# Kernel tuning notes

Hardware: AMD Instinct MI355X
Metric: run time of the kernel (lower is better)

Reference implementation:

```python
import jax, jax.numpy as jnp
import numpy as np

N = 100000   # nodes
E = 600000   # directed edges (no self loops)
T = 128      # n_timestamps
DIMS = [128, 64, 32, 16]  # get_layer_dims(128, 3, 0.5)


def _glorot(key, din, dout):
    lim = float(np.sqrt(6.0 / (din + dout)))
    return jax.random.uniform(key, (din, dout), jnp.float32, -lim, lim)


def setup_inputs() -> dict:
    key = jax.random.key(0)
    ks = jax.random.split(key, 16)
    row = jax.random.randint(ks[0], (E,), 0, N, dtype=jnp.int32)
    off = jax.random.randint(ks[1], (E,), 1, N, dtype=jnp.int32)
    col = (row + off) % N  # guarantees no self loops
    edge_index = jnp.stack([row, col])
    x = jax.random.normal(ks[2], (N, T), dtype=jnp.float32)
    enc = [(DIMS[0], DIMS[1]), (DIMS[1], DIMS[2]), (DIMS[2], DIMS[3])]
    dec = [(DIMS[3], DIMS[2]), (DIMS[2], DIMS[1]), (DIMS[1], DIMS[0])]
    inp = {"x": x, "edge_index": edge_index}
    for i, (di, do) in enumerate(enc):
        inp[f"We{i+1}"] = _glorot(ks[3 + i], di, do)
        inp[f"be{i+1}"] = 0.01 * jax.random.normal(ks[6 + i], (do,), jnp.float32)
    for i, (di, do) in enumerate(dec):
        inp[f"Wd{i+1}"] = _glorot(ks[9 + i], di, do)
        inp[f"bd{i+1}"] = 0.01 * jax.random.normal(ks[12 + i], (do,), jnp.float32)
    return inp


def _with_self_loops(edge_index, n):
    ar = jnp.arange(n, dtype=edge_index.dtype)
    row = jnp.concatenate([edge_index[0], ar])
    col = jnp.concatenate([edge_index[1], ar])
    return row, col


def _deg_inv_sqrt(w, col, n):
    deg = jax.ops.segment_sum(w, col, num_segments=n)
    return jnp.where(deg > 0, jax.lax.rsqrt(deg), 0.0)


def _smooth_norm(edge_index, n):
    # gcn_norm: A_hat = A + I (fill 1), sym normalize D^-1/2 A_hat D^-1/2
    row, col = _with_self_loops(edge_index, n)
    w = jnp.ones(row.shape[0], jnp.float32)
    dinv = _deg_inv_sqrt(w, col, n)
    return row, col, dinv[row] * w * dinv[col]


def _sharp_norm(edge_index, n):
    # gcn_sharp: A_hat = -A + 2I, D_hat from (A + 2I), norm = D^-1/2 A_hat D^-1/2
    row, col = _with_self_loops(edge_index, n)
    e = edge_index.shape[1]
    wA = jnp.concatenate([-jnp.ones(e, jnp.float32), 2.0 * jnp.ones(n, jnp.float32)])
    wD = jnp.concatenate([jnp.ones(e, jnp.float32), 2.0 * jnp.ones(n, jnp.float32)])
    dinv = _deg_inv_sqrt(wD, col, n)
    return row, col, dinv[row] * wA * dinv[col]


def _conv(x, W, b, row, col, ew, n):
    # x -> lin -> gather source, scale by edge weight, scatter-add to target, + bias
    h = x @ W
    out = jax.ops.segment_sum(ew[:, None] * h[row], col, num_segments=n)
    return out + b


def reference(x, edge_index, We1, be1, We2, be2, We3, be3,
              Wd1, bd1, Wd2, bd2, Wd3, bd3):
    n = x.shape[0]
    sr, sc, sw = _smooth_norm(edge_index, n)   # encoder ('smooth')
    hr, hc, hw = _sharp_norm(edge_index, n)    # decoder ('sharp')
    # encoder: conv+ReLU x3
    h = jax.nn.relu(_conv(x, We1, be1, sr, sc, sw, n))
    h = jax.nn.relu(_conv(h, We2, be2, sr, sc, sw, n))
    z = jax.nn.relu(_conv(h, We3, be3, sr, sc, sw, n))
    # decoder: conv+ReLU x2, final conv without ReLU
    h = jax.nn.relu(_conv(z, Wd1, bd1, hr, hc, hw, n))
    h = jax.nn.relu(_conv(h, Wd2, bd2, hr, hc, hw, n))
    o = _conv(h, Wd3, bd3, hr, hc, hw, n)
    return o
```

## Files before the change

kernel.cpp:

```cpp
#include <hip/hip_runtime.h>


static inline int ceil_div(int a, int b) { return (a + b - 1) / b; }

#define SCAN_BLK 256
#define NBINS 128

typedef _Float16 f16;
typedef _Float16 f16x8 __attribute__((ext_vector_type(8)));
typedef float f32x4 __attribute__((ext_vector_type(4)));


__global__ void zero_kernel(int* __restrict__ p, int n) {
    int i = blockIdx.x * blockDim.x + threadIdx.x;
    if (i < n) p[i] = 0;
}


__global__ void deg_kernel(const int* __restrict__ col, int* __restrict__ deg, int E) {
    int e = blockIdx.x * blockDim.x + threadIdx.x;
    if (e < E) atomicAdd(&deg[col[e]], 1);
}


__global__ void hist_kernel(const int* __restrict__ deg, int* __restrict__ blockhist, int n) {
    __shared__ int lh[NBINS];
    if (threadIdx.x < NBINS) lh[threadIdx.x] = 0;
    __syncthreads();
    int i = blockIdx.x * SCAN_BLK + threadIdx.x;
    if (i < n) {
        int d = deg[i]; if (d >= NBINS) d = NBINS - 1;
        atomicAdd(&lh[d], 1);
    }
    __syncthreads();
    if (threadIdx.x < NBINS) blockhist[blockIdx.x * NBINS + threadIdx.x] = lh[threadIdx.x];
}

__global__ void binscan_kernel(int* __restrict__ blockhist, int* __restrict__ bintot, int nb) {
    __shared__ int s[512];
    int bin = blockIdx.x, t = threadIdx.x;
    int v = (t < nb) ? blockhist[t * NBINS + bin] : 0;
    s[t] = v;
    __syncthreads();
    for (int st = 1; st < 512; st <<= 1) {
        int a = (t >= st) ? s[t - st] : 0;
        __syncthreads();
        s[t] += a;
        __syncthreads();
    }
    if (t < nb) blockhist[t * NBINS + bin] = s[t] - v;
    if (t == 0) bintot[bin] = s[511];
}

__global__ void base_scan_kernel(const int* __restrict__ bintot, int* __restrict__ binbase,
                                 int* __restrict__ edgebase) {
    __shared__ int s[NBINS], se[NBINS];
    int t = threadIdx.x;
    int v = bintot[t];
    int ve = v * t;
    s[t] = v; se[t] = ve;
    __syncthreads();
    for (int st = 1; st < NBINS; st <<= 1) {
        int a = (t >= st) ? s[t - st] : 0;
        int ae = (t >= st) ? se[t - st] : 0;
        __syncthreads();
        s[t] += a; se[t] += ae;
        __syncthreads();
    }
    binbase[t] = s[t] - v;
    edgebase[t] = se[t] - ve;
}

__global__ void place_kernel(const int* __restrict__ deg, const int* __restrict__ blockhist,
                             const int* __restrict__ binbase, int* __restrict__ order,
                             int* __restrict__ slotof, int n) {
    __shared__ int lh[NBINS];
    if (threadIdx.x < NBINS) lh[threadIdx.x] = 0;
    __syncthreads();
    int i = blockIdx.x * SCAN_BLK + threadIdx.x;
    if (i < n) {
        int d = deg[i]; if (d >= NBINS) d = NBINS - 1;
        int r = atomicAdd(&lh[d], 1);
        int slot = binbase[d] + blockhist[blockIdx.x * NBINS + d] + r;
        order[slot] = i;
        slotof[i] = slot;
    }
}

__global__ void dinvp_offs_kernel(const int* __restrict__ deg, const int* __restrict__ order,
                                  const int* __restrict__ binbase, const int* __restrict__ edgebase,
                                  float* __restrict__ dinv_s, float* __restrict__ dinv_h,
                                  int* __restrict__ offs, int* __restrict__ cursor, int n, int E) {
    int s = blockIdx.x * blockDim.x + threadIdx.x;
    if (s < n) {
        int dd = deg[order[s]];
        float d = (float)dd;
        dinv_s[s] = rsqrtf(d + 1.0f);
        dinv_h[s] = rsqrtf(d + 2.0f);
        int o = edgebase[dd] + dd * (s - binbase[dd]);
        offs[s] = o;
        cursor[s] = o;
        if (s == 0) offs[n] = E;
    }
}

__global__ void csr_fill_kernel(const int* __restrict__ row, const int* __restrict__ col,
                                const int* __restrict__ slotof, int* __restrict__ cursor,
                                int* __restrict__ src, int E) {
    int e = blockIdx.x * blockDim.x + threadIdx.x;
    if (e >= E) return;
    int cs = slotof[col[e]];
    int p = atomicAdd(&cursor[cs], 1);
    src[p] = slotof[row[e]];
}


struct WPtrs { const float* p[6]; };

__global__ void wsplit_kernel(WPtrs wp, f16* __restrict__ wt_hi, f16* __restrict__ wt_lo) {
    const int din[6]  = {128, 64, 32, 16, 32, 64};
    const int dout[6] = {64, 32, 16, 32, 64, 128};
    const int off[6]  = {0, 8192, 10240, 10752, 11264, 13312};
    int t = blockIdx.x * blockDim.x + threadIdx.x;
    if (t >= 21504) return;
    int l = 0;
    while (l < 5 && t >= off[l + 1]) ++l;
    int idx = t - off[l];
    int c = idx / din[l], k = idx - c * din[l];
    float a = wp.p[l][k * dout[l] + c];
    f16 hi = (f16)a;
    f16 lo = (f16)(a - (float)hi);
    wt_hi[t] = hi;
    wt_lo[t] = lo;
}


#define M_PLAIN 0
#define M_SMOOTH 1
#define M_SHARP 2
#define M_SHARP_RELU 3

template <int DIN, int DOUT, int WAVES, int MODE, bool ADD_BIAS, bool RELU_OUT,
          bool SCALE_ROW, bool IN_PERM, bool OUT_PERM, bool OUT_F32>
__global__ __launch_bounds__(WAVES * 64) void gemm_fused(
        const float* __restrict__ Af, const f16* __restrict__ U,
        const f16* __restrict__ Wth, const f16* __restrict__ Wtl,
        const float* __restrict__ gbias, const float* __restrict__ gdinv,
        const int* __restrict__ offs, const int* __restrict__ srcv,
        const float* __restrict__ bias, const float* __restrict__ rs,
        const int* __restrict__ map, float* __restrict__ outf,
        f16* __restrict__ outh, int n) {
    constexpr int THREADS = WAVES * 64;
    constexpr int BM   = WAVES * 16;
    constexpr int KROW = (DIN < 32) ? 32 : DIN;
    constexpr int NKC  = KROW / 32;
    constexpr int NT   = DOUT / 16;
    constexpr int LDA  = KROW * 2 + 16;
    constexpr int LDW  = 80;
    constexpr int AGF  = KROW / 8;
    __shared__ __align__(16) unsigned char lds[(size_t)BM * LDA + (size_t)2 * DOUT * LDW];
    unsigned char* Asm = lds;
    unsigned char* Wh  = lds + (size_t)BM * LDA;
    unsigned char* Wl  = Wh + (size_t)DOUT * LDW;

    const int row0 = blockIdx.x * BM;
    const int lane = threadIdx.x & 63;
    const int wave = __builtin_amdgcn_readfirstlane((int)(threadIdx.x >> 6));
    const int l15 = lane & 15, lhi = lane >> 4;

    f32x4 acc[NT];
#pragma unroll
    for (int t = 0; t < NT; ++t) acc[t] = (f32x4){0.f, 0.f, 0.f, 0.f};

    for (int i = threadIdx.x; i < BM * AGF; i += THREADS) {
        int r = i / AGF, j = i % AGF;
        f16x8 hv = {0, 0, 0, 0, 0, 0, 0, 0};
        int gr = row0 + r;
        const int k8 = j * 8;
        if (gr < n && k8 < DIN) {
            if (MODE == M_PLAIN) {
                int ar = IN_PERM ? map[gr] : gr;
                float4 v0 = *(const float4*)(Af + (size_t)ar * DIN + k8);
                float4 v1 = *(const float4*)(Af + (size_t)ar * DIN + k8 + 4);
                hv[0] = (f16)v0.x; hv[1] = (f16)v0.y; hv[2] = (f16)v0.z; hv[3] = (f16)v0.w;
                hv[4] = (f16)v1.x; hv[5] = (f16)v1.y; hv[6] = (f16)v1.z; hv[7] = (f16)v1.w;
            } else {
                f16x8 s8 = *(const f16x8*)(U + (size_t)gr * DIN + k8);
                float sf[8], g[8];
#pragma unroll
                for (int q = 0; q < 8; ++q) {
                    sf[q] = (float)s8[q];
                    if (MODE == M_SHARP_RELU) sf[q] = fmaxf(sf[q], 0.f);
                    g[q] = 0.f;
                }
                int e = offs[gr], e1 = offs[gr + 1];
                if (e < e1) {
                    const int last = e1 - 1;
                    for (; e < e1; e += 4) {
                        int i1 = (e + 1 < last) ? e + 1 : last;
                        int i2 = (e + 2 < last) ? e + 2 : last;
                        int i3 = (e + 3 < last) ? e + 3 : last;
                        int r0 = srcv[e], r1 = srcv[i1], r2 = srcv[i2], r3 = srcv[i3];
                        f16x8 t0 = *(const f16x8*)(U + (size_t)r0 * DIN + k8);
                        f16x8 t1 = *(const f16x8*)(U + (size_t)r1 * DIN + k8);
                        f16x8 t2 = *(const f16x8*)(U + (size_t)r2 * DIN + k8);
                        f16x8 t3 = *(const f16x8*)(U + (size_t)r3 * DIN + k8);
                        bool m1 = (e + 1 < e1), m2 = (e + 2 < e1), m3 = (e + 3 < e1);
#pragma unroll
                        for (int q = 0; q < 8; ++q) {
                            float a0 = (float)t0[q];
                            float a1 = (float)t1[q];
                            float a2 = (float)t2[q];
                            float a3 = (float)t3[q];
                            if (MODE == M_SHARP_RELU) {
                                a0 = fmaxf(a0, 0.f); a1 = fmaxf(a1, 0.f);
                                a2 = fmaxf(a2, 0.f); a3 = fmaxf(a3, 0.f);
                            }
                            a1 = m1 ? a1 : 0.f;
                            a2 = m2 ? a2 : 0.f;
                            a3 = m3 ? a3 : 0.f;
                            g[q] += (a0 + a1) + (a2 + a3);
                        }
                    }
                }
                float dv = gdinv[gr];
#pragma unroll
                for (int q = 0; q < 8; ++q) {
                    float v;
                    if (MODE == M_SMOOTH) {
                        v = fmaf(dv, g[q] + sf[q], gbias[k8 + q]);
                        v = fmaxf(v, 0.f);
                    } else {
                        v = dv * (2.f * sf[q] - g[q]);
                    }
                    hv[q] = (f16)v;
                }
            }
        }
        *(f16x8*)(Asm + (size_t)r * LDA + j * 16) = hv;
    }

    for (int kc = 0; kc < NKC; ++kc) {
        const int kofs = kc * 32;
        if (kc > 0) __syncthreads();
        for (int i = threadIdx.x; i < DOUT * 4; i += THREADS) {
            int c = i / 4, j = i % 4;
            f16x8 h8 = {0, 0, 0, 0, 0, 0, 0, 0}, l8 = {0, 0, 0, 0, 0, 0, 0, 0};
            if (kofs + j * 8 < DIN) {
                h8 = *(const f16x8*)(Wth + (size_t)c * DIN + kofs + j * 8);
                l8 = *(const f16x8*)(Wtl + (size_t)c * DIN + kofs + j * 8);
            }
            *(f16x8*)(Wh + (size_t)c * LDW + j * 16) = h8;
            *(f16x8*)(Wl + (size_t)c * LDW + j * 16) = l8;
        }
        __syncthreads();

        f16x8 a = *(const f16x8*)(Asm + (size_t)(wave * 16 + l15) * LDA + kc * 64 + lhi * 16);
#pragma unroll
        for (int t = 0; t < NT; ++t) {
            f16x8 bh = *(const f16x8*)(Wh + (size_t)(t * 16 + l15) * LDW + lhi * 16);
            f16x8 bl = *(const f16x8*)(Wl + (size_t)(t * 16 + l15) * LDW + lhi * 16);
            acc[t] = __builtin_amdgcn_mfma_f32_16x16x32_f16(a, bh, acc[t], 0, 0, 0);
            acc[t] = __builtin_amdgcn_mfma_f32_16x16x32_f16(a, bl, acc[t], 0, 0, 0);
        }
    }

    const int rbase = row0 + wave * 16 + (lhi << 2);
    float rsv[4]; int om[4];
#pragma unroll
    for (int r = 0; r < 4; ++r) {
        int row = rbase + r;
        bool ok = row < n;
        rsv[r] = (SCALE_ROW && ok) ? rs[row] : 1.0f;
        om[r] = ok ? (OUT_PERM ? map[row] : row) : -1;
    }
#pragma unroll
    for (int t = 0; t < NT; ++t) {
        int colb = t * 16 + l15;
        float b = ADD_BIAS ? bias[colb] : 0.f;
#pragma unroll
        for (int r = 0; r < 4; ++r) {
            if (om[r] < 0) continue;
            float v = acc[t][r] + b;
            if (RELU_OUT) v = fmaxf(v, 0.f);
            if (SCALE_ROW) v *= rsv[r];
            if (OUT_F32) outf[(size_t)om[r] * DOUT + colb] = v;
            else         outh[(size_t)om[r] * DOUT + colb] = (f16)v;
        }
    }
}


__global__ __launch_bounds__(256) void gather16(
        const f16* __restrict__ u, const int* __restrict__ offs,
        const int* __restrict__ src, const float* __restrict__ dinv,
        const float* __restrict__ ps, const float* __restrict__ bias,
        f16* __restrict__ out, int n) {
    int idx = blockIdx.x * blockDim.x + threadIdx.x;
    int node = idx >> 1;
    if (node >= n) return;
    int d8 = (idx & 1) * 8;

    f16x8 s8 = *(const f16x8*)(u + (size_t)node * 16 + d8);
    float g[8];
#pragma unroll
    for (int q = 0; q < 8; ++q) g[q] = 0.f;
    int e = offs[node], e1 = offs[node + 1];
    if (e < e1) {
        const int last = e1 - 1;
        for (; e < e1; e += 4) {
            int i1 = (e + 1 < last) ? e + 1 : last;
            int i2 = (e + 2 < last) ? e + 2 : last;
            int i3 = (e + 3 < last) ? e + 3 : last;
            int r0 = src[e], r1 = src[i1], r2 = src[i2], r3 = src[i3];
            f16x8 t0 = *(const f16x8*)(u + (size_t)r0 * 16 + d8);
            f16x8 t1 = *(const f16x8*)(u + (size_t)r1 * 16 + d8);
            f16x8 t2 = *(const f16x8*)(u + (size_t)r2 * 16 + d8);
            f16x8 t3 = *(const f16x8*)(u + (size_t)r3 * 16 + d8);
            bool m1 = (e + 1 < e1), m2 = (e + 2 < e1), m3 = (e + 3 < e1);
#pragma unroll
            for (int q = 0; q < 8; ++q) {
                float a0 = (float)t0[q];
                float a1 = m1 ? (float)t1[q] : 0.f;
                float a2 = m2 ? (float)t2[q] : 0.f;
                float a3 = m3 ? (float)t3[q] : 0.f;
                g[q] += (a0 + a1) + (a2 + a3);
            }
        }
    }
    float dv = dinv[node], p = ps[node];
    f16x8 o;
#pragma unroll
    for (int q = 0; q < 8; ++q) {
        float v = p * (fmaf(dv, g[q] + (float)s8[q], bias[d8 + q]));
        o[q] = (f16)v;
    }
    *(f16x8*)(out + (size_t)node * 16 + d8) = o;
}


extern "C" void kernel_launch(void* const* d_in, const int* in_sizes, int n_in,
                              void* d_out, int out_size, void* d_ws, size_t ws_size,
                              hipStream_t stream) {
    const int T = 128;
    const int n = in_sizes[0] / T;
    const int E = in_sizes[1] / 2;

    const float* x   = (const float*)d_in[0];
    const int* eidx  = (const int*)d_in[1];
    const int* row   = eidx;
    const int* col   = eidx + E;
    const float* We1 = (const float*)d_in[2];
    const float* be1 = (const float*)d_in[3];
    const float* We2 = (const float*)d_in[4];
    const float* be2 = (const float*)d_in[5];
    const float* We3 = (const float*)d_in[6];
    const float* be3 = (const float*)d_in[7];
    const float* Wd1 = (const float*)d_in[8];
    const float* bd1 = (const float*)d_in[9];
    const float* Wd2 = (const float*)d_in[10];
    const float* bd2 = (const float*)d_in[11];
    const float* Wd3 = (const float*)d_in[12];
    const float* bd3 = (const float*)d_in[13];
    float* out = (float*)d_out;

    char* base = (char*)d_ws;
    int*   deg      = (int*)base;   base += (size_t)n * 4;
    int*   offs     = (int*)base;   base += (size_t)(n + 4) * 4;
    int*   cursor   = (int*)base;   base += (size_t)(n + 4) * 4;
    int*   bhist    = (int*)base;   base += (size_t)512 * NBINS * 4;
    int*   bintot   = (int*)base;   base += (size_t)NBINS * 4;
    int*   binbase  = (int*)base;   base += (size_t)NBINS * 4;
    int*   edgebase = (int*)base;   base += (size_t)NBINS * 4;
    int*   order    = (int*)base;   base += (size_t)n * 4;
    int*   slotof   = (int*)base;   base += (size_t)n * 4;
    float* dinv_s   = (float*)base; base += (size_t)n * 4;
    float* dinv_h   = (float*)base; base += (size_t)n * 4;
    int*   src      = (int*)base;   base += (size_t)E * 4;
    f16*   wt_hi    = (f16*)base;   base += (size_t)21504 * 2 + 64;
    f16*   wt_lo    = (f16*)base;   base += (size_t)21504 * 2 + 64;
    f16*   bufA     = (f16*)base;   base += (size_t)n * 64 * 2;
    f16*   bufB     = (f16*)base;   base += (size_t)n * 64 * 2;
    (void)ws_size;

    const int BLK = 256;
    const int nhb = ceil_div(n, SCAN_BLK);

    zero_kernel<<<ceil_div(n, BLK), BLK, 0, stream>>>(deg, n);
    deg_kernel<<<ceil_div(E, BLK), BLK, 0, stream>>>(col, deg, E);

    hist_kernel<<<nhb, SCAN_BLK, 0, stream>>>(deg, bhist, n);
    binscan_kernel<<<NBINS, 512, 0, stream>>>(bhist, bintot, nhb);
    base_scan_kernel<<<1, NBINS, 0, stream>>>(bintot, binbase, edgebase);
    place_kernel<<<nhb, SCAN_BLK, 0, stream>>>(deg, bhist, binbase, order, slotof, n);
    dinvp_offs_kernel<<<ceil_div(n, BLK), BLK, 0, stream>>>(
        deg, order, binbase, edgebase, dinv_s, dinv_h, offs, cursor, n, E);
    csr_fill_kernel<<<ceil_div(E, BLK), BLK, 0, stream>>>(row, col, slotof, cursor, src, E);

    WPtrs wp; wp.p[0] = We1; wp.p[1] = We2; wp.p[2] = We3;
    wp.p[3] = Wd1; wp.p[4] = Wd2; wp.p[5] = Wd3;
    wsplit_kernel<<<ceil_div(21504, BLK), BLK, 0, stream>>>(wp, wt_hi, wt_lo);

    const int ggrid = ceil_div(n, 128);

    gemm_fused<128, 64, 8, M_PLAIN, false, false, true, true, false, false>
        <<<ggrid, 512, 0, stream>>>(
        x, nullptr, wt_hi + 0, wt_lo + 0, nullptr, nullptr, nullptr, nullptr,
        nullptr, dinv_s, order, nullptr, bufA, n);

    gemm_fused<64, 32, 8, M_SMOOTH, false, false, true, false, false, false>
        <<<ggrid, 512, 0, stream>>>(
        nullptr, bufA, wt_hi + 8192, wt_lo + 8192, be1, dinv_s, offs, src,
        nullptr, dinv_s, nullptr, nullptr, bufB, n);

    gemm_fused<32, 16, 8, M_SMOOTH, false, false, true, false, false, false>
        <<<ggrid, 512, 0, stream>>>(
        nullptr, bufB, wt_hi + 10240, wt_lo + 10240, be2, dinv_s, offs, src,
        nullptr, dinv_s, nullptr, nullptr, bufA, n);

    gather16<<<ceil_div(n * 2, BLK), BLK, 0, stream>>>(
        bufA, offs, src, dinv_s, dinv_h, be3, bufB, n);

    gemm_fused<16, 32, 8, M_SHARP_RELU, true, true, true, false, false, false>
        <<<ggrid, 512, 0, stream>>>(
        nullptr, bufB, wt_hi + 10752, wt_lo + 10752, nullptr, dinv_h, offs, src,
        bd1, dinv_h, nullptr, nullptr, bufA, n);

    gemm_fused<32, 64, 8, M_SHARP, true, true, true, false, false, false>
        <<<ggrid, 512, 0, stream>>>(
        nullptr, bufA, wt_hi + 11264, wt_lo + 11264, nullptr, dinv_h, offs, src,
        bd2, dinv_h, nullptr, nullptr, bufB, n);

    gemm_fused<64, 128, 8, M_SHARP, true, false, false, false, true, true>
        <<<ggrid, 512, 0, stream>>>(
        nullptr, bufB, wt_hi + 13312, wt_lo + 13312, nullptr, dinv_h, offs, src,
        bd3, nullptr, order, out, nullptr, n);
}
```

Baseline: 219.5 us.

## Fuse CSR offset setup into placement and widen per-thread neighbor gathers

The separate dinv/offset kernel is folded into place_kernel, so per-slot degree normalisers, CSR offsets and cursors are written right where each node's slot is assigned. This removes one launch and the indirect deg[order[s]] read. In the fused GEMM prologue and in gather16, each thread now handles 16 feature halves of a row instead of 8. That halves the number of redundant edge-index loads and offset reads per row and issues more independent vector loads per thread. The cost is fewer active threads, higher register pressure, and idle threads in the DIN=16 layer.

```diff
diff --git a/kernel.cpp b/kernel.cpp
--- a/kernel.cpp
+++ b/kernel.cpp
@@ -72,35 +72,28 @@
 }
 
 __global__ void place_kernel(const int* __restrict__ deg, const int* __restrict__ blockhist,
-                             const int* __restrict__ binbase, int* __restrict__ order,
-                             int* __restrict__ slotof, int n) {
+                             const int* __restrict__ binbase, const int* __restrict__ edgebase,
+                             int* __restrict__ order, int* __restrict__ slotof,
+                             float* __restrict__ dinv_s, float* __restrict__ dinv_h,
+                             int* __restrict__ offs, int* __restrict__ cursor, int n, int E) {
     __shared__ int lh[NBINS];
     if (threadIdx.x < NBINS) lh[threadIdx.x] = 0;
     __syncthreads();
     int i = blockIdx.x * SCAN_BLK + threadIdx.x;
     if (i < n) {
-        int d = deg[i]; if (d >= NBINS) d = NBINS - 1;
-        int r = atomicAdd(&lh[d], 1);
-        int slot = binbase[d] + blockhist[blockIdx.x * NBINS + d] + r;
+        int dd = deg[i];
+        int b = dd < NBINS ? dd : NBINS - 1;
+        int r = atomicAdd(&lh[b], 1);
+        int slot = binbase[b] + blockhist[blockIdx.x * NBINS + b] + r;
         order[slot] = i;
         slotof[i] = slot;
-    }
-}
-
-__global__ void dinvp_offs_kernel(const int* __restrict__ deg, const int* __restrict__ order,
-                                  const int* __restrict__ binbase, const int* __restrict__ edgebase,
-                                  float* __restrict__ dinv_s, float* __restrict__ dinv_h,
-                                  int* __restrict__ offs, int* __restrict__ cursor, int n, int E) {
-    int s = blockIdx.x * blockDim.x + threadIdx.x;
-    if (s < n) {
-        int dd = deg[order[s]];
         float d = (float)dd;
-        dinv_s[s] = rsqrtf(d + 1.0f);
-        dinv_h[s] = rsqrtf(d + 2.0f);
-        int o = edgebase[dd] + dd * (s - binbase[dd]);
-        offs[s] = o;
-        cursor[s] = o;
-        if (s == 0) offs[n] = E;
+        dinv_s[slot] = rsqrtf(d + 1.0f);
+        dinv_h[slot] = rsqrtf(d + 2.0f);
+        int o = edgebase[dd] + dd * (slot - binbase[dd]);
+        offs[slot] = o;
+        cursor[slot] = o;
+        if (i == 0) offs[n] = E;
     }
 }
 
@@ -157,7 +150,7 @@
     constexpr int NT   = DOUT / 16;
     constexpr int LDA  = KROW * 2 + 16;
     constexpr int LDW  = 80;
-    constexpr int AGF  = KROW / 8;
+    constexpr int NP   = KROW / 16;
     __shared__ __align__(16) unsigned char lds[(size_t)BM * LDA + (size_t)2 * DOUT * LDW];
     unsigned char* Asm = lds;
     unsigned char* Wh  = lds + (size_t)BM * LDA;
@@ -172,24 +165,36 @@
 #pragma unroll
     for (int t = 0; t < NT; ++t) acc[t] = (f32x4){0.f, 0.f, 0.f, 0.f};
 
-    for (int i = threadIdx.x; i < BM * AGF; i += THREADS) {
-        int r = i / AGF, j = i % AGF;
-        f16x8 hv = {0, 0, 0, 0, 0, 0, 0, 0};
+    for (int i = threadIdx.x; i < BM * NP; i += THREADS) {
+        int r = i / NP, jp = i % NP;
+        f16x8 hv0 = {0, 0, 0, 0, 0, 0, 0, 0};
+        f16x8 hv1 = {0, 0, 0, 0, 0, 0, 0, 0};
         int gr = row0 + r;
-        const int k8 = j * 8;
-        if (gr < n && k8 < DIN) {
+        const int k16 = jp * 16;
+        if (gr < n && k16 < DIN) {
             if (MODE == M_PLAIN) {
                 int ar = IN_PERM ? map[gr] : gr;
-                float4 v0 = *(const float4*)(Af + (size_t)ar * DIN + k8);
-                float4 v1 = *(const float4*)(Af + (size_t)ar * DIN + k8 + 4);
-                hv[0] = (f16)v0.x; hv[1] = (f16)v0.y; hv[2] = (f16)v0.z; hv[3] = (f16)v0.w;
-                hv[4] = (f16)v1.x; hv[5] = (f16)v1.y; hv[6] = (f16)v1.z; hv[7] = (f16)v1.w;
+                const float* ap = Af + (size_t)ar * DIN + k16;
+                float4 v0 = *(const float4*)(ap);
+                float4 v1 = *(const float4*)(ap + 4);
+                float4 v2 = *(const float4*)(ap + 8);
+                float4 v3 = *(const float4*)(ap + 12);
+                hv0[0] = (f16)v0.x; hv0[1] = (f16)v0.y; hv0[2] = (f16)v0.z; hv0[3] = (f16)v0.w;
+                hv0[4] = (f16)v1.x; hv0[5] = (f16)v1.y; hv0[6] = (f16)v1.z; hv0[7] = (f16)v1.w;
+                hv1[0] = (f16)v2.x; hv1[1] = (f16)v2.y; hv1[2] = (f16)v2.z; hv1[3] = (f16)v2.w;
+                hv1[4] = (f16)v3.x; hv1[5] = (f16)v3.y; hv1[6] = (f16)v3.z; hv1[7] = (f16)v3.w;
             } else {
-                f16x8 s8 = *(const f16x8*)(U + (size_t)gr * DIN + k8);
-                float sf[8], g[8];
+                const f16* ub = U + (size_t)gr * DIN + k16;
+                f16x8 sa = *(const f16x8*)(ub);
+                f16x8 sb = *(const f16x8*)(ub + 8);
+                float sf[16], g[16];
 #pragma unroll
                 for (int q = 0; q < 8; ++q) {
-                    sf[q] = (float)s8[q];
+                    sf[q] = (float)sa[q];
+                    sf[q + 8] = (float)sb[q];
+                }
+#pragma unroll
+                for (int q = 0; q < 16; ++q) {
                     if (MODE == M_SHARP_RELU) sf[q] = fmaxf(sf[q], 0.f);
                     g[q] = 0.f;
                 }
@@ -201,43 +206,53 @@
                         int i2 = (e + 2 < last) ? e + 2 : last;
                         int i3 = (e + 3 < last) ? e + 3 : last;
                         int r0 = srcv[e], r1 = srcv[i1], r2 = srcv[i2], r3 = srcv[i3];
-                        f16x8 t0 = *(const f16x8*)(U + (size_t)r0 * DIN + k8);
-                        f16x8 t1 = *(const f16x8*)(U + (size_t)r1 * DIN + k8);
-                        f16x8 t2 = *(const f16x8*)(U + (size_t)r2 * DIN + k8);
-                        f16x8 t3 = *(const f16x8*)(U + (size_t)r3 * DIN + k8);
+                        const f16* p0 = U + (size_t)r0 * DIN + k16;
+                        const f16* p1 = U + (size_t)r1 * DIN + k16;
+                        const f16* p2 = U + (size_t)r2 * DIN + k16;
+                        const f16* p3 = U + (size_t)r3 * DIN + k16;
+                        f16x8 t0a = *(const f16x8*)(p0), t0b = *(const f16x8*)(p0 + 8);
+                        f16x8 t1a = *(const f16x8*)(p1), t1b = *(const f16x8*)(p1 + 8);
+                        f16x8 t2a = *(const f16x8*)(p2), t2b = *(const f16x8*)(p2 + 8);
+                        f16x8 t3a = *(const f16x8*)(p3), t3b = *(const f16x8*)(p3 + 8);
                         bool m1 = (e + 1 < e1), m2 = (e + 2 < e1), m3 = (e + 3 < e1);
 #pragma unroll
                         for (int q = 0; q < 8; ++q) {
-                            float a0 = (float)t0[q];
-                            float a1 = (float)t1[q];
-                            float a2 = (float)t2[q];
-                            float a3 = (float)t3[q];
+                            float a0 = (float)t0a[q], b0 = (float)t0b[q];
+                            float a1 = (float)t1a[q], b1 = (float)t1b[q];
+                            float a2 = (float)t2a[q], b2 = (float)t2b[q];
+                            float a3 = (float)t3a[q], b3 = (float)t3b[q];
                             if (MODE == M_SHARP_RELU) {
                                 a0 = fmaxf(a0, 0.f); a1 = fmaxf(a1, 0.f);
                                 a2 = fmaxf(a2, 0.f); a3 = fmaxf(a3, 0.f);
+                                b0 = fmaxf(b0, 0.f); b1 = fmaxf(b1, 0.f);
+                                b2 = fmaxf(b2, 0.f); b3 = fmaxf(b3, 0.f);
                             }
-                            a1 = m1 ? a1 : 0.f;
-                            a2 = m2 ? a2 : 0.f;
-                            a3 = m3 ? a3 : 0.f;
+                            a1 = m1 ? a1 : 0.f; b1 = m1 ? b1 : 0.f;
+                            a2 = m2 ? a2 : 0.f; b2 = m2 ? b2 : 0.f;
+                            a3 = m3 ? a3 : 0.f; b3 = m3 ? b3 : 0.f;
                             g[q] += (a0 + a1) + (a2 + a3);
+                            g[q + 8] += (b0 + b1) + (b2 + b3);
                         }
                     }
                 }
                 float dv = gdinv[gr];
 #pragma unroll
-                for (int q = 0; q < 8; ++q) {
+                for (int q = 0; q < 16; ++q) {
                     float v;
                     if (MODE == M_SMOOTH) {
-                        v = fmaf(dv, g[q] + sf[q], gbias[k8 + q]);
+                        v = fmaf(dv, g[q] + sf[q], gbias[k16 + q]);
                         v = fmaxf(v, 0.f);
                     } else {
                         v = dv * (2.f * sf[q] - g[q]);
                     }
-                    hv[q] = (f16)v;
+                    if (q < 8) hv0[q] = (f16)v;
+                    else       hv1[q - 8] = (f16)v;
                 }
             }
         }
-        *(f16x8*)(Asm + (size_t)r * LDA + j * 16) = hv;
+        unsigned char* dst = Asm + (size_t)r * LDA + jp * 32;
+        *(f16x8*)(dst) = hv0;
+        *(f16x8*)(dst + 16) = hv1;
     }
 
     for (int kc = 0; kc < NKC; ++kc) {
@@ -296,15 +311,15 @@
         const int* __restrict__ src, const float* __restrict__ dinv,
         const float* __restrict__ ps, const float* __restrict__ bias,
         f16* __restrict__ out, int n) {
-    int idx = blockIdx.x * blockDim.x + threadIdx.x;
-    int node = idx >> 1;
+    int node = blockIdx.x * blockDim.x + threadIdx.x;
     if (node >= n) return;
-    int d8 = (idx & 1) * 8;
-
-    f16x8 s8 = *(const f16x8*)(u + (size_t)node * 16 + d8);
-    float g[8];
-#pragma unroll
-    for (int q = 0; q < 8; ++q) g[q] = 0.f;
+
+    const f16* ub = u + (size_t)node * 16;
+    f16x8 sa = *(const f16x8*)(ub);
+    f16x8 sb = *(const f16x8*)(ub + 8);
+    float g[16];
+#pragma unroll
+    for (int q = 0; q < 16; ++q) g[q] = 0.f;
     int e = offs[node], e1 = offs[node + 1];
     if (e < e1) {
         const int last = e1 - 1;
@@ -313,29 +328,36 @@
             int i2 = (e + 2 < last) ? e + 2 : last;
             int i3 = (e + 3 < last) ? e + 3 : last;
             int r0 = src[e], r1 = src[i1], r2 = src[i2], r3 = src[i3];
-            f16x8 t0 = *(const f16x8*)(u + (size_t)r0 * 16 + d8);
-            f16x8 t1 = *(const f16x8*)(u + (size_t)r1 * 16 + d8);
-            f16x8 t2 = *(const f16x8*)(u + (size_t)r2 * 16 + d8);
-            f16x8 t3 = *(const f16x8*)(u + (size_t)r3 * 16 + d8);
+            const f16* p0 = u + (size_t)r0 * 16;
+            const f16* p1 = u + (size_t)r1 * 16;
+            const f16* p2 = u + (size_t)r2 * 16;
+            const f16* p3 = u + (size_t)r3 * 16;
+            f16x8 t0a = *(const f16x8*)(p0), t0b = *(const f16x8*)(p0 + 8);
+            f16x8 t1a = *(const f16x8*)(p1), t1b = *(const f16x8*)(p1 + 8);
+            f16x8 t2a = *(const f16x8*)(p2), t2b = *(const f16x8*)(p2 + 8);
+            f16x8 t3a = *(const f16x8*)(p3), t3b = *(const f16x8*)(p3 + 8);
             bool m1 = (e + 1 < e1), m2 = (e + 2 < e1), m3 = (e + 3 < e1);
 #pragma unroll
             for (int q = 0; q < 8; ++q) {
-                float a0 = (float)t0[q];
-                float a1 = m1 ? (float)t1[q] : 0.f;
-                float a2 = m2 ? (float)t2[q] : 0.f;
-                float a3 = m3 ? (float)t3[q] : 0.f;
+                float a0 = (float)t0a[q], b0 = (float)t0b[q];
+                float a1 = m1 ? (float)t1a[q] : 0.f, b1 = m1 ? (float)t1b[q] : 0.f;
+                float a2 = m2 ? (float)t2a[q] : 0.f, b2 = m2 ? (float)t2b[q] : 0.f;
+                float a3 = m3 ? (float)t3a[q] : 0.f, b3 = m3 ? (float)t3b[q] : 0.f;
                 g[q] += (a0 + a1) + (a2 + a3);
+                g[q + 8] += (b0 + b1) + (b2 + b3);
             }
         }
     }
     float dv = dinv[node], p = ps[node];
-    f16x8 o;
+    f16x8 oa, ob;
 #pragma unroll
     for (int q = 0; q < 8; ++q) {
-        float v = p * (fmaf(dv, g[q] + (float)s8[q], bias[d8 + q]));
-        o[q] = (f16)v;
-    }
-    *(f16x8*)(out + (size_t)node * 16 + d8) = o;
+        oa[q] = (f16)(p * fmaf(dv, g[q] + (float)sa[q], bias[q]));
+        ob[q] = (f16)(p * fmaf(dv, g[q + 8] + (float)sb[q], bias[q + 8]));
+    }
+    f16* ob_ptr = out + (size_t)node * 16;
+    *(f16x8*)(ob_ptr) = oa;
+    *(f16x8*)(ob_ptr + 8) = ob;
 }
 
 
@@ -392,9 +414,8 @@
     hist_kernel<<<nhb, SCAN_BLK, 0, stream>>>(deg, bhist, n);
     binscan_kernel<<<NBINS, 512, 0, stream>>>(bhist, bintot, nhb);
     base_scan_kernel<<<1, NBINS, 0, stream>>>(bintot, binbase, edgebase);
-    place_kernel<<<nhb, SCAN_BLK, 0, stream>>>(deg, bhist, binbase, order, slotof, n);
-    dinvp_offs_kernel<<<ceil_div(n, BLK), BLK, 0, stream>>>(
-        deg, order, binbase, edgebase, dinv_s, dinv_h, offs, cursor, n, E);
+    place_kernel<<<nhb, SCAN_BLK, 0, stream>>>(
+        deg, bhist, binbase, edgebase, order, slotof, dinv_s, dinv_h, offs, cursor, n, E);
     csr_fill_kernel<<<ceil_div(E, BLK), BLK, 0, stream>>>(row, col, slotof, cursor, src, E);
 
     WPtrs wp; wp.p[0] = We1; wp.p[1] = We2; wp.p[2] = We3;
@@ -418,7 +439,7 @@
         nullptr, bufB, wt_hi + 10240, wt_lo + 10240, be2, dinv_s, offs, src,
         nullptr, dinv_s, nullptr, nullptr, bufA, n);
 
-    gather16<<<ceil_div(n * 2, BLK), BLK, 0, stream>>>(
+    gather16<<<ceil_div(n, BLK), BLK, 0, stream>>>(
         bufA, offs, src, dinv_s, dinv_h, be3, bufB, n);
 
     gemm_fused<16, 32, 8, M_SHARP_RELU, true, true, true, false, false, false>
```

Result: slower. 241.6 us (+10.0%).

## Fuse degree-normalization/offset setup into placement and unroll edge gathers by eight

Applied to the files above, without the earlier changes.

Merges the dinv/offset computation into place_kernel so slot, dinv and CSR offsets are written in one pass, removing one kernel launch and the indirect deg[order[s]] lookup. Separately, the neighbor-gather loops in the fused GEMM and gather16 kernels now process eight edges per iteration instead of four, to raise the number of outstanding loads. With average degree around six, the wider unroll issues more redundant clamped loads and uses more registers, which may cut occupancy.

```diff
diff --git a/kernel.cpp b/kernel.cpp
--- a/kernel.cpp
+++ b/kernel.cpp
@@ -72,35 +72,28 @@
 }
 
 __global__ void place_kernel(const int* __restrict__ deg, const int* __restrict__ blockhist,
-                             const int* __restrict__ binbase, int* __restrict__ order,
-                             int* __restrict__ slotof, int n) {
+                             const int* __restrict__ binbase, const int* __restrict__ edgebase,
+                             int* __restrict__ order, int* __restrict__ slotof,
+                             float* __restrict__ dinv_s, float* __restrict__ dinv_h,
+                             int* __restrict__ offs, int* __restrict__ cursor, int n, int E) {
     __shared__ int lh[NBINS];
     if (threadIdx.x < NBINS) lh[threadIdx.x] = 0;
     __syncthreads();
     int i = blockIdx.x * SCAN_BLK + threadIdx.x;
     if (i < n) {
-        int d = deg[i]; if (d >= NBINS) d = NBINS - 1;
-        int r = atomicAdd(&lh[d], 1);
-        int slot = binbase[d] + blockhist[blockIdx.x * NBINS + d] + r;
+        int dd = deg[i];
+        int b = dd < NBINS ? dd : NBINS - 1;
+        int r = atomicAdd(&lh[b], 1);
+        int slot = binbase[b] + blockhist[blockIdx.x * NBINS + b] + r;
         order[slot] = i;
         slotof[i] = slot;
-    }
-}
-
-__global__ void dinvp_offs_kernel(const int* __restrict__ deg, const int* __restrict__ order,
-                                  const int* __restrict__ binbase, const int* __restrict__ edgebase,
-                                  float* __restrict__ dinv_s, float* __restrict__ dinv_h,
-                                  int* __restrict__ offs, int* __restrict__ cursor, int n, int E) {
-    int s = blockIdx.x * blockDim.x + threadIdx.x;
-    if (s < n) {
-        int dd = deg[order[s]];
         float d = (float)dd;
-        dinv_s[s] = rsqrtf(d + 1.0f);
-        dinv_h[s] = rsqrtf(d + 2.0f);
-        int o = edgebase[dd] + dd * (s - binbase[dd]);
-        offs[s] = o;
-        cursor[s] = o;
-        if (s == 0) offs[n] = E;
+        dinv_s[slot] = rsqrtf(d + 1.0f);
+        dinv_h[slot] = rsqrtf(d + 2.0f);
+        int o = edgebase[dd] + dd * (slot - binbase[dd]);
+        offs[slot] = o;
+        cursor[slot] = o;
+        if (i == 0) offs[n] = E;
     }
 }
 
@@ -196,30 +189,43 @@
                 int e = offs[gr], e1 = offs[gr + 1];
                 if (e < e1) {
                     const int last = e1 - 1;
-                    for (; e < e1; e += 4) {
+                    for (; e < e1; e += 8) {
                         int i1 = (e + 1 < last) ? e + 1 : last;
                         int i2 = (e + 2 < last) ? e + 2 : last;
                         int i3 = (e + 3 < last) ? e + 3 : last;
-                        int r0 = srcv[e], r1 = srcv[i1], r2 = srcv[i2], r3 = srcv[i3];
+                        int i4 = (e + 4 < last) ? e + 4 : last;
+                        int i5 = (e + 5 < last) ? e + 5 : last;
+                        int i6 = (e + 6 < last) ? e + 6 : last;
+                        int i7 = (e + 7 < last) ? e + 7 : last;
+                        int r0 = srcv[e],  r1 = srcv[i1], r2 = srcv[i2], r3 = srcv[i3];
+                        int r4 = srcv[i4], r5 = srcv[i5], r6 = srcv[i6], r7 = srcv[i7];
                         f16x8 t0 = *(const f16x8*)(U + (size_t)r0 * DIN + k8);
                         f16x8 t1 = *(const f16x8*)(U + (size_t)r1 * DIN + k8);
                         f16x8 t2 = *(const f16x8*)(U + (size_t)r2 * DIN + k8);
                         f16x8 t3 = *(const f16x8*)(U + (size_t)r3 * DIN + k8);
+                        f16x8 t4 = *(const f16x8*)(U + (size_t)r4 * DIN + k8);
+                        f16x8 t5 = *(const f16x8*)(U + (size_t)r5 * DIN + k8);
+                        f16x8 t6 = *(const f16x8*)(U + (size_t)r6 * DIN + k8);
+                        f16x8 t7 = *(const f16x8*)(U + (size_t)r7 * DIN + k8);
                         bool m1 = (e + 1 < e1), m2 = (e + 2 < e1), m3 = (e + 3 < e1);
+                        bool m4 = (e + 4 < e1), m5 = (e + 5 < e1), m6 = (e + 6 < e1);
+                        bool m7 = (e + 7 < e1);
 #pragma unroll
                         for (int q = 0; q < 8; ++q) {
                             float a0 = (float)t0[q];
-                            float a1 = (float)t1[q];
-                            float a2 = (float)t2[q];
-                            float a3 = (float)t3[q];
+                            float a1 = (float)t1[q], a2 = (float)t2[q], a3 = (float)t3[q];
+                            float a4 = (float)t4[q], a5 = (float)t5[q], a6 = (float)t6[q];
+                            float a7 = (float)t7[q];
                             if (MODE == M_SHARP_RELU) {
                                 a0 = fmaxf(a0, 0.f); a1 = fmaxf(a1, 0.f);
                                 a2 = fmaxf(a2, 0.f); a3 = fmaxf(a3, 0.f);
+                                a4 = fmaxf(a4, 0.f); a5 = fmaxf(a5, 0.f);
+                                a6 = fmaxf(a6, 0.f); a7 = fmaxf(a7, 0.f);
                             }
-                            a1 = m1 ? a1 : 0.f;
-                            a2 = m2 ? a2 : 0.f;
-                            a3 = m3 ? a3 : 0.f;
-                            g[q] += (a0 + a1) + (a2 + a3);
+                            a1 = m1 ? a1 : 0.f; a2 = m2 ? a2 : 0.f; a3 = m3 ? a3 : 0.f;
+                            a4 = m4 ? a4 : 0.f; a5 = m5 ? a5 : 0.f; a6 = m6 ? a6 : 0.f;
+                            a7 = m7 ? a7 : 0.f;
+                            g[q] += ((a0 + a1) + (a2 + a3)) + ((a4 + a5) + (a6 + a7));
                         }
                     }
                 }
@@ -308,23 +314,38 @@
     int e = offs[node], e1 = offs[node + 1];
     if (e < e1) {
         const int last = e1 - 1;
-        for (; e < e1; e += 4) {
+        for (; e < e1; e += 8) {
             int i1 = (e + 1 < last) ? e + 1 : last;
             int i2 = (e + 2 < last) ? e + 2 : last;
             int i3 = (e + 3 < last) ? e + 3 : last;
-            int r0 = src[e], r1 = src[i1], r2 = src[i2], r3 = src[i3];
+            int i4 = (e + 4 < last) ? e + 4 : last;
+            int i5 = (e + 5 < last) ? e + 5 : last;
+            int i6 = (e + 6 < last) ? e + 6 : last;
+            int i7 = (e + 7 < last) ? e + 7 : last;
+            int r0 = src[e],  r1 = src[i1], r2 = src[i2], r3 = src[i3];
+            int r4 = src[i4], r5 = src[i5], r6 = src[i6], r7 = src[i7];
             f16x8 t0 = *(const f16x8*)(u + (size_t)r0 * 16 + d8);
             f16x8 t1 = *(const f16x8*)(u + (size_t)r1 * 16 + d8);
             f16x8 t2 = *(const f16x8*)(u + (size_t)r2 * 16 + d8);
             f16x8 t3 = *(const f16x8*)(u + (size_t)r3 * 16 + d8);
+            f16x8 t4 = *(const f16x8*)(u + (size_t)r4 * 16 + d8);
+            f16x8 t5 = *(const f16x8*)(u + (size_t)r5 * 16 + d8);
+            f16x8 t6 = *(const f16x8*)(u + (size_t)r6 * 16 + d8);
+            f16x8 t7 = *(const f16x8*)(u + (size_t)r7 * 16 + d8);
             bool m1 = (e + 1 < e1), m2 = (e + 2 < e1), m3 = (e + 3 < e1);
+            bool m4 = (e + 4 < e1), m5 = (e + 5 < e1), m6 = (e + 6 < e1);
+            bool m7 = (e + 7 < e1);
 #pragma unroll
             for (int q = 0; q < 8; ++q) {
                 float a0 = (float)t0[q];
                 float a1 = m1 ? (float)t1[q] : 0.f;
                 float a2 = m2 ? (float)t2[q] : 0.f;
                 float a3 = m3 ? (float)t3[q] : 0.f;
-                g[q] += (a0 + a1) + (a2 + a3);
+                float a4 = m4 ? (float)t4[q] : 0.f;
+                float a5 = m5 ? (float)t5[q] : 0.f;
+                float a6 = m6 ? (float)t6[q] : 0.f;
+                float a7 = m7 ? (float)t7[q] : 0.f;
+                g[q] += ((a0 + a1) + (a2 + a3)) + ((a4 + a5) + (a6 + a7));
             }
         }
     }
@@ -392,9 +413,8 @@
     hist_kernel<<<nhb, SCAN_BLK, 0, stream>>>(deg, bhist, n);
     binscan_kernel<<<NBINS, 512, 0, stream>>>(bhist, bintot, nhb);
     base_scan_kernel<<<1, NBINS, 0, stream>>>(bintot, binbase, edgebase);
-    place_kernel<<<nhb, SCAN_BLK, 0, stream>>>(deg, bhist, binbase, order, slotof, n);
-    dinvp_offs_kernel<<<ceil_div(n, BLK), BLK, 0, stream>>>(
-        deg, order, binbase, edgebase, dinv_s, dinv_h, offs, cursor, n, E);
+    place_kernel<<<nhb, SCAN_BLK, 0, stream>>>(
+        deg, bhist, binbase, edgebase, order, slotof, dinv_s, dinv_h, offs, cursor, n, E);
     csr_fill_kernel<<<ceil_div(E, BLK), BLK, 0, stream>>>(row, col, slotof, cursor, src, E);
 
     WPtrs wp; wp.p[0] = We1; wp.p[1] = We2; wp.p[2] = We3;
```

Result: slower. 233.8 us (+6.5%).
